# Optimization experiments

Hardware: AMD Instinct MI355X
Metric: run time of the kernel (lower is better)

Reference implementation:

```python
import jax, jax.numpy as jnp
import numpy as np

B, N, T, D, M, HOPS = 32, 300, 12, 64, 16, 2

def setup_inputs() -> dict:
    key = jax.random.key(0)
    ks = jax.random.split(key, 12)
    inp = {
        "X": jax.random.normal(ks[0], (B, D, N, T), dtype=jnp.float32),
        "timeEmbedding": jax.random.normal(ks[1], (B, N, T, D), dtype=jnp.float32),
        "adjW": jax.random.normal(ks[2], (N, D), dtype=jnp.float32) * (1.0 / np.sqrt(D)),
        "adjB": jnp.zeros((N,), dtype=jnp.float32),
        "trainW1": jax.random.normal(ks[3], (N, M), dtype=jnp.float32) * 0.1,
        "trainW2": jax.random.normal(ks[4], (M, D * D), dtype=jnp.float32) * 0.1,
        "alpha1": jax.random.normal(ks[5], (N, M), dtype=jnp.float32) * 0.1,
        "alpha2": jax.random.normal(ks[6], (M, N), dtype=jnp.float32) * 0.1,
        "beta1": jax.random.normal(ks[7], (N, M), dtype=jnp.float32) * 0.1,
        "beta2": jax.random.normal(ks[8], (M, N), dtype=jnp.float32) * 0.1,
        "gcnW": jax.random.normal(ks[9], (D, D * (HOPS + 1)), dtype=jnp.float32) * (1.0 / np.sqrt(D * (HOPS + 1))),
        "gcnB": jnp.zeros((D,), dtype=jnp.float32),
    }
    return inp

def reference(X, timeEmbedding, adjW, adjB, trainW1, trainW2, alpha1, alpha2, beta1, beta2, gcnW, gcnB):
    # timeEmbedding: [B,N,T,D] -> [B,T,N,D]
    te = jnp.transpose(timeEmbedding, (0, 2, 1, 3))
    # learned adjacency: A[b,t,n,k]
    A = jnp.sin(jnp.einsum('btnd,kd->btnk', te, adjW) + adjB)  # Linear(dmodel->N)
    A = (alpha1 @ alpha2) * A            # elementwise scale by [N,N], broadcast over b,t
    A = jax.nn.relu(A + beta1 @ beta2)
    # X: [B,D,N,T] -> [B,T,N,D]
    Xp = jnp.transpose(X, (0, 3, 2, 1))
    # per-node weight matrices [N,D,D]
    W = (trainW1 @ trainW2).reshape(N, D, D)
    Hs = [Xp]
    Hb = Xp
    for _ in range(HOPS):
        Hnow = jnp.einsum('btnk,btkd->btnd', A, Hb)      # adjacency aggregation
        Hnow = jnp.einsum('btnk,nkd->btnd', Hnow, W)     # per-node distinct matmul
        pre = Xp + Hnow
        Hnow = jax.nn.sigmoid(pre) * jnp.tanh(pre)        # gated residual
        Hs.append(Hnow)
        Hb = Hnow
    H = jnp.concatenate(Hs, axis=3)                       # [B,T,N,D*(hops+1)]
    Hout = jnp.einsum('btnf,df->btnd', H, gcnW) + gcnB    # gcnLinear (dropout = identity in eval)
    return jnp.transpose(Hout, (0, 3, 2, 1))              # [B,D,N,T]
```

## Files before the change

kernel.cpp:

```cpp
#include <hip/hip_runtime.h>

#define Nq 300
#define Tq 12
#define Dq 64
#define Mq 16
#define BTq 384
#define DDq (Dq*Dq)
#define Fq (Dq*3)
#define NP 320

typedef short bf8_t __attribute__((ext_vector_type(8)));
typedef float f4_t  __attribute__((ext_vector_type(4)));

__device__ __forceinline__ unsigned short f2bf(float f) {
    unsigned u = __float_as_uint(f);
    u = (u + 0x7FFFu + ((u >> 16) & 1u)) >> 16;
    return (unsigned short)u;
}
__device__ __forceinline__ float bf2f(unsigned short u) {
    return __uint_as_float((unsigned)u << 16);
}
__device__ __forceinline__ float4 ld4(const float* p) { return *(const float4*)p; }

__device__ __forceinline__ bf8_t pack8(float4 a, float4 b) {
    bf8_t r;
    r[0] = (short)f2bf(a.x); r[1] = (short)f2bf(a.y);
    r[2] = (short)f2bf(a.z); r[3] = (short)f2bf(a.w);
    r[4] = (short)f2bf(b.x); r[5] = (short)f2bf(b.y);
    r[6] = (short)f2bf(b.z); r[7] = (short)f2bf(b.w);
    return r;
}

__device__ __forceinline__ float gatef(float p) {
    float pc = fminf(fmaxf(p, -30.f), 30.f);
    float sig = 1.f / (1.f + __expf(-pc));
    float e2  = __expf(2.f * pc);
    float th  = (e2 - 1.f) / (e2 + 1.f);
    return sig * th;
}

__global__ void __launch_bounds__(256) kprep_all(
    const float* __restrict__ a1, const float* __restrict__ a2,
    const float* __restrict__ b1, const float* __restrict__ b2,
    const float* __restrict__ w1, const float* __restrict__ w2,
    const float* __restrict__ adjW, const float* __restrict__ adjB,
    const float* __restrict__ X,
    unsigned* __restrict__ ABt, unsigned short* __restrict__ Wt,
    unsigned short* __restrict__ adjWb, float* __restrict__ adjBp,
    unsigned short* __restrict__ Xp_t, unsigned short* __restrict__ Xp_nb)
{
    __shared__ char smem[64 * 308 * 2];
    const int vb = blockIdx.x;
    const int tid = threadIdx.x;

    if (vb < 400) {
        const int tile = vb;
        const int reg = tid & 3, lane = tid >> 2;
        const int nt = tile % 5;  int r1 = tile / 5;
        const int w  = r1 % 4;    int r2 = r1 / 4;
        const int c  = r2 % 5;    const int qi = r2 / 5;
        const int n = qi*80 + nt*16 + (lane & 15);
        const int k = c*64 + w*16 + (lane >> 4)*4 + reg;
        unsigned outv = 0u;
        if (n < Nq && k < Nq) {
            float sa = 0.f, sb = 0.f;
            #pragma unroll
            for (int m = 0; m < Mq; ++m) {
                sa = fmaf(a1[n*Mq+m], a2[m*Nq+k], sa);
                sb = fmaf(b1[n*Mq+m], b2[m*Nq+k], sb);
            }
            outv = ((unsigned)f2bf(sb) << 16) | (unsigned)f2bf(sa);
        }
        ABt[tile*256 + tid] = outv;
    } else if (vb < 700) {
        float* sT = (float*)smem;
        __shared__ float sw1[Mq];
        const int n = vb - 400;
        if (tid < Mq) sw1[tid] = w1[n*Mq + tid];
        __syncthreads();
        for (int i = tid; i < DDq; i += 256) {
            int k = i >> 6, d = i & 63;
            float s = 0.f;
            #pragma unroll
            for (int m = 0; m < Mq; ++m) s = fmaf(sw1[m], w2[m*DDq + i], s);
            sT[d*65 + k] = s;
        }
        __syncthreads();
        for (int i = tid; i < DDq; i += 256) {
            int d = i >> 6, k = i & 63;
            Wt[(size_t)n*DDq + i] = f2bf(sT[d*65 + k]);
        }
    } else if (vb < 780) {
        int e = (vb - 700) * 256 + tid;
        if (e < NP * 64) {
            int k = e >> 6, d = e & 63;
            adjWb[e] = (k < Nq) ? f2bf(adjW[k*Dq + d]) : (unsigned short)0;
        }
        if (e < NP) adjBp[e] = (e < Nq) ? adjB[e] : 0.f;
    } else {
        unsigned short* sT = (unsigned short*)smem;
        const int bx = vb - 780;
        const int b = bx / 12, tile = bx % 12;
        const int n0 = tile * 25;
        for (int i = tid; i < 64 * 300; i += 256) {
            int d = i / 300, j = i - d * 300;
            sT[d*308 + j] = f2bf(X[(size_t)(b*64 + d)*3600 + n0*12 + j]);
        }
        __syncthreads();
        for (int wi = tid; wi < 12 * 64 * 25; wi += 256) {
            int nl = wi % 25, rem = wi / 25;
            int d = rem % 64, t = rem / 64;
            Xp_t[((size_t)(b*Tq + t)*64 + d)*NP + n0 + nl] = sT[d*308 + nl*12 + t];
        }
        if (tile == 11) {
            for (int wi = tid; wi < 12 * 64 * 20; wi += 256) {
                int e = wi % 20, rem = wi / 20;
                int d = rem % 64, t = rem / 64;
                Xp_t[((size_t)(b*Tq + t)*64 + d)*NP + 300 + e] = 0;
            }
        }
        for (int wi = tid; wi < 25 * 12 * 64; wi += 256) {
            int d = wi & 63, rem = wi >> 6;
            int t = rem % 12, nl = rem / 12;
            Xp_nb[((size_t)(n0 + nl)*BTq + b*Tq + t)*64 + d] = sT[d*308 + nl*12 + t];
        }
    }
}

__global__ void __launch_bounds__(256) ktr2(const unsigned short* __restrict__ Hnb,
                                            unsigned short* __restrict__ Ht) {
    __shared__ unsigned short sT[64 * 308];
    const int bt = blockIdx.x;
    const int tid = threadIdx.x;
    for (int i = tid; i < 300 * 64; i += 256) {
        int n = i >> 6, d = i & 63;
        sT[d*308 + n] = Hnb[((size_t)n*BTq + bt)*64 + d];
    }
    __syncthreads();
    for (int wi = tid; wi < 64 * 80; wi += 256) {
        int kq = wi % 80, d = wi / 80;
        ushort4 o;
        int k = kq * 4;
        o.x = (k+0 < Nq) ? sT[d*308 + k+0] : (unsigned short)0;
        o.y = (k+1 < Nq) ? sT[d*308 + k+1] : (unsigned short)0;
        o.z = (k+2 < Nq) ? sT[d*308 + k+2] : (unsigned short)0;
        o.w = (k+3 < Nq) ? sT[d*308 + k+3] : (unsigned short)0;
        *(ushort4*)&Ht[((size_t)bt*64 + d)*NP + k] = o;
    }
}

__global__ void __launch_bounds__(256) kfuse(
    const float* __restrict__ te,
    const unsigned short* __restrict__ adjWb,
    const float* __restrict__ adjBp,
    const unsigned* __restrict__ ABt,
    const unsigned short* __restrict__ Hb_t,
    unsigned short* __restrict__ Hout_nb)
{
    __shared__ unsigned short sPl[2][80 * 72];
    const int bt = blockIdx.x >> 2, qi = blockIdx.x & 3;
    const int b = bt / Tq, t = bt - b * Tq;
    const int nbase = qi * 80;
    const int tid = threadIdx.x;
    const int w = tid >> 6, lane = tid & 63, quad = lane >> 4, l16 = lane & 15;
    const int dcol = w*16 + l16;

    bf8_t tb0[5], tb1[5];
    #pragma unroll
    for (int nt = 0; nt < 5; ++nt) {
        int n = nbase + nt*16 + l16; if (n > Nq-1) n = Nq-1;
        const float* ter = te + (((size_t)b*Nq + n)*Tq + t)*Dq;
        tb0[nt] = pack8(ld4(ter + quad*8),      ld4(ter + quad*8 + 4));
        tb1[nt] = pack8(ld4(ter + 32 + quad*8), ld4(ter + 36 + quad*8));
    }
    f4_t accO[5];
    #pragma unroll
    for (int rt = 0; rt < 5; ++rt) accO[rt] = (f4_t){0.f, 0.f, 0.f, 0.f};

    for (int c = 0; c < 5; ++c) {
        const int cbase = c * 64;
        const unsigned short* ar = adjWb + (cbase + w*16 + l16)*64;
        bf8_t ka0 = *(const bf8_t*)(ar + quad*8);
        bf8_t ka1 = *(const bf8_t*)(ar + 32 + quad*8);
        float4 bias4 = ld4(adjBp + cbase + w*16 + quad*4);
        const unsigned* abbase = ABt + ((((size_t)qi*5 + c)*4 + w)*5)*256 + lane*4;
        unsigned short* sp = sPl[c & 1];
        #pragma unroll
        for (int nt = 0; nt < 5; ++nt) {
            f4_t p = {0.f, 0.f, 0.f, 0.f};
            p = __builtin_amdgcn_mfma_f32_16x16x32_bf16(ka0, tb0[nt], p, 0, 0, 0);
            p = __builtin_amdgcn_mfma_f32_16x16x32_bf16(ka1, tb1[nt], p, 0, 0, 0);
            uint4 ab = *(const uint4*)(abbase + nt*256);
            ushort4 o4;
            {
                float sv = __sinf(p[0] + bias4.x);
                o4.x = f2bf(fmaxf(fmaf(__uint_as_float(ab.x << 16), sv,
                                       __uint_as_float(ab.x & 0xFFFF0000u)), 0.f));
            }
            {
                float sv = __sinf(p[1] + bias4.y);
                o4.y = f2bf(fmaxf(fmaf(__uint_as_float(ab.y << 16), sv,
                                       __uint_as_float(ab.y & 0xFFFF0000u)), 0.f));
            }
            {
                float sv = __sinf(p[2] + bias4.z);
                o4.z = f2bf(fmaxf(fmaf(__uint_as_float(ab.z << 16), sv,
                                       __uint_as_float(ab.z & 0xFFFF0000u)), 0.f));
            }
            {
                float sv = __sinf(p[3] + bias4.w);
                o4.w = f2bf(fmaxf(fmaf(__uint_as_float(ab.w << 16), sv,
                                       __uint_as_float(ab.w & 0xFFFF0000u)), 0.f));
            }
            *(ushort4*)&sp[(nt*16 + l16)*72 + w*16 + quad*4] = o4;
        }
        __syncthreads();
        const unsigned short* hr = Hb_t + ((size_t)bt*64 + dcol)*NP + cbase;
        bf8_t v0 = *(const bf8_t*)(hr + quad*8);
        bf8_t v1 = *(const bf8_t*)(hr + 32 + quad*8);
        #pragma unroll
        for (int rt = 0; rt < 5; ++rt) {
            bf8_t p0 = *(const bf8_t*)&sp[(rt*16 + l16)*72 + quad*8];
            bf8_t p1 = *(const bf8_t*)&sp[(rt*16 + l16)*72 + 32 + quad*8];
            accO[rt] = __builtin_amdgcn_mfma_f32_16x16x32_bf16(p0, v0, accO[rt], 0, 0, 0);
            accO[rt] = __builtin_amdgcn_mfma_f32_16x16x32_bf16(p1, v1, accO[rt], 0, 0, 0);
        }
    }
    #pragma unroll
    for (int rt = 0; rt < 5; ++rt) {
        #pragma unroll
        for (int reg = 0; reg < 4; ++reg) {
            int ng = nbase + rt*16 + quad*4 + reg;
            if (ng < Nq)
                Hout_nb[((size_t)ng*BTq + bt)*64 + dcol] = f2bf(accO[rt][reg]);
        }
    }
}

__global__ void __launch_bounds__(256) kmm(
    const unsigned short* __restrict__ Hagg_nb,
    const unsigned short* __restrict__ Xp_nb,
    const unsigned short* __restrict__ Wt,
    unsigned short* __restrict__ Hout_nb)
{
    const int n = blockIdx.x >> 2, qi = blockIdx.x & 3;
    const int bt0 = qi * 96;
    const int tid = threadIdx.x;
    const int w = tid >> 6, lane = tid & 63, quad = lane >> 4, l16 = lane & 15;
    const int dcol = w*16 + l16;
    const unsigned short* wn = Wt + (size_t)n * DDq + dcol*64;
    bf8_t v0 = *(const bf8_t*)(wn + quad*8);
    bf8_t v1 = *(const bf8_t*)(wn + 32 + quad*8);
    f4_t acc[6];
    #pragma unroll
    for (int rt = 0; rt < 6; ++rt) acc[rt] = (f4_t){0.f, 0.f, 0.f, 0.f};
    #pragma unroll
    for (int rt = 0; rt < 6; ++rt) {
        int r = bt0 + rt*16 + l16;
        const unsigned short* row = Hagg_nb + ((size_t)n*BTq + r)*64;
        bf8_t a0 = *(const bf8_t*)(row + quad*8);
        bf8_t a1 = *(const bf8_t*)(row + 32 + quad*8);
        acc[rt] = __builtin_amdgcn_mfma_f32_16x16x32_bf16(a0, v0, acc[rt], 0, 0, 0);
        acc[rt] = __builtin_amdgcn_mfma_f32_16x16x32_bf16(a1, v1, acc[rt], 0, 0, 0);
    }
    __syncthreads();
    #pragma unroll
    for (int rt = 0; rt < 6; ++rt) {
        #pragma unroll
        for (int reg = 0; reg < 4; ++reg) {
            int r = bt0 + rt*16 + quad*4 + reg;
            size_t idx = ((size_t)n*BTq + r)*64 + dcol;
            float xp = bf2f(Xp_nb[idx]);
            Hout_nb[idx] = f2bf(gatef(xp + acc[rt][reg]));
        }
    }
}

__global__ void __launch_bounds__(256) kgcn(
    const unsigned short* __restrict__ Xp_nb, const unsigned short* __restrict__ H1_nb,
    const unsigned short* __restrict__ H2_nb, const float* __restrict__ gcnW,
    const float* __restrict__ gcnB, float* __restrict__ out)
{
    const int b = blockIdx.x / 19, tile = blockIdx.x % 19;
    const int n0 = tile * 16;
    const int rows = (tile == 18) ? 144 : 192;
    const int tid = threadIdx.x;
    const int w = tid >> 6, lane = tid & 63, quad = lane >> 4, l16 = lane & 15;
    const int dcol = w*16 + l16;
    const float bias = gcnB[dcol];
    f4_t acc[12];
    #pragma unroll
    for (int rt = 0; rt < 12; ++rt) acc[rt] = (f4_t){0.f, 0.f, 0.f, 0.f};
    const unsigned short* bufs[3] = {Xp_nb, H1_nb, H2_nb};
    #pragma unroll
    for (int c = 0; c < 3; ++c) {
        const unsigned short* buf = bufs[c];
        const float* gwr = gcnW + (size_t)dcol*Fq + c*Dq;
        bf8_t v0 = pack8(ld4(gwr + quad*8),      ld4(gwr + quad*8 + 4));
        bf8_t v1 = pack8(ld4(gwr + 32 + quad*8), ld4(gwr + 36 + quad*8));
        #pragma unroll
        for (int rt = 0; rt < 12; ++rt) {
            int r = rt*16 + l16;
            int nl = r / 12, t = r - nl*12;
            int n = n0 + nl; if (n > Nq-1) n = Nq-1;
            const unsigned short* row = buf + ((size_t)n*BTq + b*Tq + t)*64;
            bf8_t a0 = *(const bf8_t*)(row + quad*8);
            bf8_t a1 = *(const bf8_t*)(row + 32 + quad*8);
            acc[rt] = __builtin_amdgcn_mfma_f32_16x16x32_bf16(a0, v0, acc[rt], 0, 0, 0);
            acc[rt] = __builtin_amdgcn_mfma_f32_16x16x32_bf16(a1, v1, acc[rt], 0, 0, 0);
        }
    }
    float* outd = out + (size_t)(b*Dq + dcol)*3600 + n0*12;
    #pragma unroll
    for (int rt = 0; rt < 12; ++rt) {
        if (rt*16 < rows) {
            int r0 = rt*16 + quad*4;
            float4 o = make_float4(acc[rt][0] + bias, acc[rt][1] + bias,
                                   acc[rt][2] + bias, acc[rt][3] + bias);
            *(float4*)&outd[r0] = o;
        }
    }
}

extern "C" void kernel_launch(void* const* d_in, const int* in_sizes, int n_in,
                              void* d_out, int out_size, void* d_ws, size_t ws_size,
                              hipStream_t stream) {
    (void)in_sizes; (void)n_in; (void)out_size; (void)ws_size;
    const float* X    = (const float*)d_in[0];
    const float* te   = (const float*)d_in[1];
    const float* adjW = (const float*)d_in[2];
    const float* adjB = (const float*)d_in[3];
    const float* w1   = (const float*)d_in[4];
    const float* w2   = (const float*)d_in[5];
    const float* a1   = (const float*)d_in[6];
    const float* a2   = (const float*)d_in[7];
    const float* b1   = (const float*)d_in[8];
    const float* b2   = (const float*)d_in[9];
    const float* gW   = (const float*)d_in[10];
    const float* gB   = (const float*)d_in[11];
    float* out = (float*)d_out;

    char* ws = (char*)d_ws;
    unsigned*       ABt    = (unsigned*)      (ws);
    unsigned short* adjWb  = (unsigned short*)(ws + 409600);
    float*          adjBp  = (float*)         (ws + 450560);
    unsigned short* Wt     = (unsigned short*)(ws + 451840);
    unsigned short* Xp_t   = (unsigned short*)(ws + 2909440);
    unsigned short* Xp_nb  = (unsigned short*)(ws + 18638080);
    unsigned short* Hagg   = (unsigned short*)(ws + 33383680);
    unsigned short* H1_nb  = (unsigned short*)(ws + 48129280);
    unsigned short* H1_t   = (unsigned short*)(ws + 62874880);

    hipLaunchKernelGGL(kprep_all, dim3(1164), dim3(256), 0, stream,
                       a1, a2, b1, b2, w1, w2, adjW, adjB, X,
                       ABt, Wt, adjWb, adjBp, Xp_t, Xp_nb);
    hipLaunchKernelGGL(kfuse, dim3(1536), dim3(256), 0, stream, te, adjWb, adjBp, ABt, Xp_t, Hagg);
    hipLaunchKernelGGL(kmm,   dim3(1200), dim3(256), 0, stream, Hagg, Xp_nb, Wt, H1_nb);
    hipLaunchKernelGGL(ktr2,  dim3(384),  dim3(256), 0, stream, H1_nb, H1_t);
    hipLaunchKernelGGL(kfuse, dim3(1536), dim3(256), 0, stream, te, adjWb, adjBp, ABt, H1_t, Hagg);
    hipLaunchKernelGGL(kmm,   dim3(1200), dim3(256), 0, stream, Hagg, Xp_nb, Wt, Hagg);
    hipLaunchKernelGGL(kgcn,  dim3(608), dim3(256), 0, stream, Xp_nb, H1_nb, Hagg, gW, gB, out);
}
```

Baseline: 324.6 us.

## Pre-convert time embedding, fuse transpose into kmm, restructure kfuse and split kgcn

The time embedding is converted to bf16 once in the prep kernel, so the two kfuse launches no longer each re-read and pack fp32 data. kfuse now builds the full adjacency tile in shared memory with a single barrier instead of one per chunk. It preloads H and swaps MFMA operands so its output stores become vectorised ushort4 writes. kmm also swaps operands for vectorised gate stores and writes the transposed H1 directly, which removes the separate ktr2 launch; those transposed writes are scattered 2-byte stores. kgcn is split into two halves per tile to double the grid, and the gate divisions use fast __fdividef.

```diff
diff --git a/kernel.cpp b/kernel.cpp
--- a/kernel.cpp
+++ b/kernel.cpp
@@ -33,9 +33,9 @@
 
 __device__ __forceinline__ float gatef(float p) {
     float pc = fminf(fmaxf(p, -30.f), 30.f);
-    float sig = 1.f / (1.f + __expf(-pc));
+    float sig = __fdividef(1.f, 1.f + __expf(-pc));
     float e2  = __expf(2.f * pc);
-    float th  = (e2 - 1.f) / (e2 + 1.f);
+    float th  = __fdividef(e2 - 1.f, e2 + 1.f);
     return sig * th;
 }
 
@@ -44,10 +44,11 @@
     const float* __restrict__ b1, const float* __restrict__ b2,
     const float* __restrict__ w1, const float* __restrict__ w2,
     const float* __restrict__ adjW, const float* __restrict__ adjB,
-    const float* __restrict__ X,
+    const float* __restrict__ X, const float* __restrict__ te,
     unsigned* __restrict__ ABt, unsigned short* __restrict__ Wt,
     unsigned short* __restrict__ adjWb, float* __restrict__ adjBp,
-    unsigned short* __restrict__ Xp_t, unsigned short* __restrict__ Xp_nb)
+    unsigned short* __restrict__ Xp_t, unsigned short* __restrict__ Xp_nb,
+    unsigned short* __restrict__ te_b, unsigned short* __restrict__ H1_t)
 {
     __shared__ char smem[64 * 308 * 2];
     const int vb = blockIdx.x;
@@ -97,7 +98,7 @@
             adjWb[e] = (k < Nq) ? f2bf(adjW[k*Dq + d]) : (unsigned short)0;
         }
         if (e < NP) adjBp[e] = (e < Nq) ? adjB[e] : 0.f;
-    } else {
+    } else if (vb < 1164) {
         unsigned short* sT = (unsigned short*)smem;
         const int bx = vb - 780;
         const int b = bx / 12, tile = bx % 12;
@@ -124,59 +125,56 @@
             int t = rem % 12, nl = rem / 12;
             Xp_nb[((size_t)(n0 + nl)*BTq + b*Tq + t)*64 + d] = sT[d*308 + nl*12 + t];
         }
-    }
-}
-
-__global__ void __launch_bounds__(256) ktr2(const unsigned short* __restrict__ Hnb,
-                                            unsigned short* __restrict__ Ht) {
-    __shared__ unsigned short sT[64 * 308];
-    const int bt = blockIdx.x;
-    const int tid = threadIdx.x;
-    for (int i = tid; i < 300 * 64; i += 256) {
-        int n = i >> 6, d = i & 63;
-        sT[d*308 + n] = Hnb[((size_t)n*BTq + bt)*64 + d];
-    }
-    __syncthreads();
-    for (int wi = tid; wi < 64 * 80; wi += 256) {
-        int kq = wi % 80, d = wi / 80;
-        ushort4 o;
-        int k = kq * 4;
-        o.x = (k+0 < Nq) ? sT[d*308 + k+0] : (unsigned short)0;
-        o.y = (k+1 < Nq) ? sT[d*308 + k+1] : (unsigned short)0;
-        o.z = (k+2 < Nq) ? sT[d*308 + k+2] : (unsigned short)0;
-        o.w = (k+3 < Nq) ? sT[d*308 + k+3] : (unsigned short)0;
-        *(ushort4*)&Ht[((size_t)bt*64 + d)*NP + k] = o;
+    } else if (vb < 1548) {
+        const int bt = vb - 1164;
+        const int b = bt / Tq, t = bt - b * Tq;
+        for (int i = tid; i < 300 * 32; i += 256) {
+            int n = i >> 5, dp = (i & 31) * 2;
+            const float* s = te + (((size_t)b*Nq + n)*Tq + t)*Dq + dp;
+            unsigned lo = f2bf(s[0]), hi = f2bf(s[1]);
+            *(unsigned*)&te_b[((size_t)bt*Nq + n)*Dq + dp] = lo | (hi << 16);
+        }
+    } else {
+        const int bt = vb - 1548;
+        for (int i = tid; i < 64 * 20; i += 256) {
+            int d = i / 20, e = i % 20;
+            H1_t[((size_t)bt*64 + d)*NP + 300 + e] = 0;
+        }
     }
 }
 
 __global__ void __launch_bounds__(256) kfuse(
-    const float* __restrict__ te,
+    const unsigned short* __restrict__ te_b,
     const unsigned short* __restrict__ adjWb,
     const float* __restrict__ adjBp,
     const unsigned* __restrict__ ABt,
     const unsigned short* __restrict__ Hb_t,
     unsigned short* __restrict__ Hout_nb)
 {
-    __shared__ unsigned short sPl[2][80 * 72];
+    __shared__ unsigned short sPl[80 * 328];
     const int bt = blockIdx.x >> 2, qi = blockIdx.x & 3;
-    const int b = bt / Tq, t = bt - b * Tq;
     const int nbase = qi * 80;
     const int tid = threadIdx.x;
     const int w = tid >> 6, lane = tid & 63, quad = lane >> 4, l16 = lane & 15;
-    const int dcol = w*16 + l16;
+    const int drow = w*16 + l16;
 
     bf8_t tb0[5], tb1[5];
     #pragma unroll
     for (int nt = 0; nt < 5; ++nt) {
         int n = nbase + nt*16 + l16; if (n > Nq-1) n = Nq-1;
-        const float* ter = te + (((size_t)b*Nq + n)*Tq + t)*Dq;
-        tb0[nt] = pack8(ld4(ter + quad*8),      ld4(ter + quad*8 + 4));
-        tb1[nt] = pack8(ld4(ter + 32 + quad*8), ld4(ter + 36 + quad*8));
-    }
-    f4_t accO[5];
-    #pragma unroll
-    for (int rt = 0; rt < 5; ++rt) accO[rt] = (f4_t){0.f, 0.f, 0.f, 0.f};
-
+        const unsigned short* r = te_b + ((size_t)bt*Nq + n)*64;
+        tb0[nt] = *(const bf8_t*)(r + quad*8);
+        tb1[nt] = *(const bf8_t*)(r + 32 + quad*8);
+    }
+    bf8_t hb0[5], hb1[5];
+    const unsigned short* hbase = Hb_t + ((size_t)bt*64 + drow)*NP;
+    #pragma unroll
+    for (int c = 0; c < 5; ++c) {
+        hb0[c] = *(const bf8_t*)(hbase + c*64 + quad*8);
+        hb1[c] = *(const bf8_t*)(hbase + c*64 + 32 + quad*8);
+    }
+
+    #pragma unroll
     for (int c = 0; c < 5; ++c) {
         const int cbase = c * 64;
         const unsigned short* ar = adjWb + (cbase + w*16 + l16)*64;
@@ -184,7 +182,6 @@
         bf8_t ka1 = *(const bf8_t*)(ar + 32 + quad*8);
         float4 bias4 = ld4(adjBp + cbase + w*16 + quad*4);
         const unsigned* abbase = ABt + ((((size_t)qi*5 + c)*4 + w)*5)*256 + lane*4;
-        unsigned short* sp = sPl[c & 1];
         #pragma unroll
         for (int nt = 0; nt < 5; ++nt) {
             f4_t p = {0.f, 0.f, 0.f, 0.f};
@@ -212,27 +209,32 @@
                 o4.w = f2bf(fmaxf(fmaf(__uint_as_float(ab.w << 16), sv,
                                        __uint_as_float(ab.w & 0xFFFF0000u)), 0.f));
             }
-            *(ushort4*)&sp[(nt*16 + l16)*72 + w*16 + quad*4] = o4;
-        }
-        __syncthreads();
-        const unsigned short* hr = Hb_t + ((size_t)bt*64 + dcol)*NP + cbase;
-        bf8_t v0 = *(const bf8_t*)(hr + quad*8);
-        bf8_t v1 = *(const bf8_t*)(hr + 32 + quad*8);
+            *(ushort4*)&sPl[(nt*16 + l16)*328 + cbase + w*16 + quad*4] = o4;
+        }
+    }
+    __syncthreads();
+
+    f4_t accO[5];
+    #pragma unroll
+    for (int rt = 0; rt < 5; ++rt) accO[rt] = (f4_t){0.f, 0.f, 0.f, 0.f};
+    #pragma unroll
+    for (int c = 0; c < 5; ++c) {
         #pragma unroll
         for (int rt = 0; rt < 5; ++rt) {
-            bf8_t p0 = *(const bf8_t*)&sp[(rt*16 + l16)*72 + quad*8];
-            bf8_t p1 = *(const bf8_t*)&sp[(rt*16 + l16)*72 + 32 + quad*8];
-            accO[rt] = __builtin_amdgcn_mfma_f32_16x16x32_bf16(p0, v0, accO[rt], 0, 0, 0);
-            accO[rt] = __builtin_amdgcn_mfma_f32_16x16x32_bf16(p1, v1, accO[rt], 0, 0, 0);
+            bf8_t p0 = *(const bf8_t*)&sPl[(rt*16 + l16)*328 + c*64 + quad*8];
+            bf8_t p1 = *(const bf8_t*)&sPl[(rt*16 + l16)*328 + c*64 + 32 + quad*8];
+            accO[rt] = __builtin_amdgcn_mfma_f32_16x16x32_bf16(hb0[c], p0, accO[rt], 0, 0, 0);
+            accO[rt] = __builtin_amdgcn_mfma_f32_16x16x32_bf16(hb1[c], p1, accO[rt], 0, 0, 0);
         }
     }
     #pragma unroll
     for (int rt = 0; rt < 5; ++rt) {
-        #pragma unroll
-        for (int reg = 0; reg < 4; ++reg) {
-            int ng = nbase + rt*16 + quad*4 + reg;
-            if (ng < Nq)
-                Hout_nb[((size_t)ng*BTq + bt)*64 + dcol] = f2bf(accO[rt][reg]);
+        int ng = nbase + rt*16 + l16;
+        if (ng < Nq) {
+            ushort4 o;
+            o.x = f2bf(accO[rt][0]); o.y = f2bf(accO[rt][1]);
+            o.z = f2bf(accO[rt][2]); o.w = f2bf(accO[rt][3]);
+            *(ushort4*)&Hout_nb[((size_t)ng*BTq + bt)*64 + w*16 + quad*4] = o;
         }
     }
 }
@@ -241,16 +243,16 @@
     const unsigned short* __restrict__ Hagg_nb,
     const unsigned short* __restrict__ Xp_nb,
     const unsigned short* __restrict__ Wt,
-    unsigned short* __restrict__ Hout_nb)
+    unsigned short* __restrict__ Hout_nb,
+    unsigned short* __restrict__ Ht)
 {
     const int n = blockIdx.x >> 2, qi = blockIdx.x & 3;
     const int bt0 = qi * 96;
     const int tid = threadIdx.x;
     const int w = tid >> 6, lane = tid & 63, quad = lane >> 4, l16 = lane & 15;
-    const int dcol = w*16 + l16;
-    const unsigned short* wn = Wt + (size_t)n * DDq + dcol*64;
-    bf8_t v0 = *(const bf8_t*)(wn + quad*8);
-    bf8_t v1 = *(const bf8_t*)(wn + 32 + quad*8);
+    const unsigned short* wn = Wt + (size_t)n * DDq + (w*16 + l16)*64;
+    bf8_t a0 = *(const bf8_t*)(wn + quad*8);
+    bf8_t a1 = *(const bf8_t*)(wn + 32 + quad*8);
     f4_t acc[6];
     #pragma unroll
     for (int rt = 0; rt < 6; ++rt) acc[rt] = (f4_t){0.f, 0.f, 0.f, 0.f};
@@ -258,20 +260,29 @@
     for (int rt = 0; rt < 6; ++rt) {
         int r = bt0 + rt*16 + l16;
         const unsigned short* row = Hagg_nb + ((size_t)n*BTq + r)*64;
-        bf8_t a0 = *(const bf8_t*)(row + quad*8);
-        bf8_t a1 = *(const bf8_t*)(row + 32 + quad*8);
-        acc[rt] = __builtin_amdgcn_mfma_f32_16x16x32_bf16(a0, v0, acc[rt], 0, 0, 0);
-        acc[rt] = __builtin_amdgcn_mfma_f32_16x16x32_bf16(a1, v1, acc[rt], 0, 0, 0);
+        bf8_t b0 = *(const bf8_t*)(row + quad*8);
+        bf8_t b1 = *(const bf8_t*)(row + 32 + quad*8);
+        acc[rt] = __builtin_amdgcn_mfma_f32_16x16x32_bf16(a0, b0, acc[rt], 0, 0, 0);
+        acc[rt] = __builtin_amdgcn_mfma_f32_16x16x32_bf16(a1, b1, acc[rt], 0, 0, 0);
     }
     __syncthreads();
+    const int dbase = w*16 + quad*4;
     #pragma unroll
     for (int rt = 0; rt < 6; ++rt) {
-        #pragma unroll
-        for (int reg = 0; reg < 4; ++reg) {
-            int r = bt0 + rt*16 + quad*4 + reg;
-            size_t idx = ((size_t)n*BTq + r)*64 + dcol;
-            float xp = bf2f(Xp_nb[idx]);
-            Hout_nb[idx] = f2bf(gatef(xp + acc[rt][reg]));
+        int r = bt0 + rt*16 + l16;
+        size_t idx = ((size_t)n*BTq + r)*64 + dbase;
+        ushort4 xp4 = *(const ushort4*)&Xp_nb[idx];
+        ushort4 o;
+        o.x = f2bf(gatef(bf2f(xp4.x) + acc[rt][0]));
+        o.y = f2bf(gatef(bf2f(xp4.y) + acc[rt][1]));
+        o.z = f2bf(gatef(bf2f(xp4.z) + acc[rt][2]));
+        o.w = f2bf(gatef(bf2f(xp4.w) + acc[rt][3]));
+        *(ushort4*)&Hout_nb[idx] = o;
+        if (Ht) {
+            Ht[((size_t)r*64 + dbase + 0)*NP + n] = o.x;
+            Ht[((size_t)r*64 + dbase + 1)*NP + n] = o.y;
+            Ht[((size_t)r*64 + dbase + 2)*NP + n] = o.z;
+            Ht[((size_t)r*64 + dbase + 3)*NP + n] = o.w;
         }
     }
 }
@@ -281,16 +292,19 @@
     const unsigned short* __restrict__ H2_nb, const float* __restrict__ gcnW,
     const float* __restrict__ gcnB, float* __restrict__ out)
 {
-    const int b = blockIdx.x / 19, tile = blockIdx.x % 19;
+    const int bx = blockIdx.x;
+    const int half = bx & 1;
+    const int bt19 = bx >> 1;
+    const int b = bt19 / 19, tile = bt19 % 19;
     const int n0 = tile * 16;
     const int rows = (tile == 18) ? 144 : 192;
     const int tid = threadIdx.x;
     const int w = tid >> 6, lane = tid & 63, quad = lane >> 4, l16 = lane & 15;
     const int dcol = w*16 + l16;
     const float bias = gcnB[dcol];
-    f4_t acc[12];
-    #pragma unroll
-    for (int rt = 0; rt < 12; ++rt) acc[rt] = (f4_t){0.f, 0.f, 0.f, 0.f};
+    f4_t acc[6];
+    #pragma unroll
+    for (int rt = 0; rt < 6; ++rt) acc[rt] = (f4_t){0.f, 0.f, 0.f, 0.f};
     const unsigned short* bufs[3] = {Xp_nb, H1_nb, H2_nb};
     #pragma unroll
     for (int c = 0; c < 3; ++c) {
@@ -299,8 +313,8 @@
         bf8_t v0 = pack8(ld4(gwr + quad*8),      ld4(gwr + quad*8 + 4));
         bf8_t v1 = pack8(ld4(gwr + 32 + quad*8), ld4(gwr + 36 + quad*8));
         #pragma unroll
-        for (int rt = 0; rt < 12; ++rt) {
-            int r = rt*16 + l16;
+        for (int rt = 0; rt < 6; ++rt) {
+            int r = half*96 + rt*16 + l16;
             int nl = r / 12, t = r - nl*12;
             int n = n0 + nl; if (n > Nq-1) n = Nq-1;
             const unsigned short* row = buf + ((size_t)n*BTq + b*Tq + t)*64;
@@ -312,9 +326,10 @@
     }
     float* outd = out + (size_t)(b*Dq + dcol)*3600 + n0*12;
     #pragma unroll
-    for (int rt = 0; rt < 12; ++rt) {
-        if (rt*16 < rows) {
-            int r0 = rt*16 + quad*4;
+    for (int rt = 0; rt < 6; ++rt) {
+        int ra = half*96 + rt*16;
+        if (ra < rows) {
+            int r0 = ra + quad*4;
             float4 o = make_float4(acc[rt][0] + bias, acc[rt][1] + bias,
                                    acc[rt][2] + bias, acc[rt][3] + bias);
             *(float4*)&outd[r0] = o;
@@ -345,19 +360,20 @@
     unsigned short* adjWb  = (unsigned short*)(ws + 409600);
     float*          adjBp  = (float*)         (ws + 450560);
     unsigned short* Wt     = (unsigned short*)(ws + 451840);
-    unsigned short* Xp_t   = (unsigned short*)(ws + 2909440);
-    unsigned short* Xp_nb  = (unsigned short*)(ws + 18638080);
-    unsigned short* Hagg   = (unsigned short*)(ws + 33383680);
-    unsigned short* H1_nb  = (unsigned short*)(ws + 48129280);
-    unsigned short* H1_t   = (unsigned short*)(ws + 62874880);
-
-    hipLaunchKernelGGL(kprep_all, dim3(1164), dim3(256), 0, stream,
-                       a1, a2, b1, b2, w1, w2, adjW, adjB, X,
-                       ABt, Wt, adjWb, adjBp, Xp_t, Xp_nb);
-    hipLaunchKernelGGL(kfuse, dim3(1536), dim3(256), 0, stream, te, adjWb, adjBp, ABt, Xp_t, Hagg);
-    hipLaunchKernelGGL(kmm,   dim3(1200), dim3(256), 0, stream, Hagg, Xp_nb, Wt, H1_nb);
-    hipLaunchKernelGGL(ktr2,  dim3(384),  dim3(256), 0, stream, H1_nb, H1_t);
-    hipLaunchKernelGGL(kfuse, dim3(1536), dim3(256), 0, stream, te, adjWb, adjBp, ABt, H1_t, Hagg);
-    hipLaunchKernelGGL(kmm,   dim3(1200), dim3(256), 0, stream, Hagg, Xp_nb, Wt, Hagg);
-    hipLaunchKernelGGL(kgcn,  dim3(608), dim3(256), 0, stream, Xp_nb, H1_nb, Hagg, gW, gB, out);
-}
+    unsigned short* te_b   = (unsigned short*)(ws + 2909440);
+    unsigned short* Xp_t   = (unsigned short*)(ws + 17655040);
+    unsigned short* Xp_nb  = (unsigned short*)(ws + 33383680);
+    unsigned short* Hagg   = (unsigned short*)(ws + 48129280);
+    unsigned short* H1_nb  = (unsigned short*)(ws + 62874880);
+    unsigned short* H1_t   = (unsigned short*)(ws + 77620480);
+
+    hipLaunchKernelGGL(kprep_all, dim3(1932), dim3(256), 0, stream,
+                       a1, a2, b1, b2, w1, w2, adjW, adjB, X, te,
+                       ABt, Wt, adjWb, adjBp, Xp_t, Xp_nb, te_b, H1_t);
+    hipLaunchKernelGGL(kfuse, dim3(1536), dim3(256), 0, stream, te_b, adjWb, adjBp, ABt, Xp_t, Hagg);
+    hipLaunchKernelGGL(kmm,   dim3(1200), dim3(256), 0, stream, Hagg, Xp_nb, Wt, H1_nb, H1_t);
+    hipLaunchKernelGGL(kfuse, dim3(1536), dim3(256), 0, stream, te_b, adjWb, adjBp, ABt, H1_t, Hagg);
+    hipLaunchKernelGGL(kmm,   dim3(1200), dim3(256), 0, stream, Hagg, Xp_nb, Wt, Hagg,
+                       (unsigned short*)nullptr);
+    hipLaunchKernelGGL(kgcn,  dim3(1216), dim3(256), 0, stream, Xp_nb, H1_nb, Hagg, gW, gB, out);
+}
```

Measured after the change: 332.2 us. 1.02x slower.
